# Kernel optimization log

Measured on AMD Instinct MI355X. Metric: run time of the kernel, lower is better.

## Reference

```python
import jax, jax.numpy as jnp
import numpy as np

_SIGMA = 1.5
_K1 = 0.01
_K2 = 0.03
_WINDOW_SIZE = 11
_N_CHANNELS = 3
_VALUE_RANGE = 1.0
_WEIGHTS = np.array([0.0448, 0.2856, 0.3001, 0.2363, 0.1333], dtype=np.float32)


def create_window(window_size: int, n_channels: int) -> jnp.ndarray:
    # 2D Gaussian kernel, normalized to sum 1, expanded to depthwise (C,1,ws,ws)
    coords = np.arange(window_size, dtype=np.float32) - (window_size - 1) / 2.0
    g = np.exp(-(coords ** 2) / (2.0 * _SIGMA ** 2))
    g = g / g.sum()
    k2d = np.outer(g, g).astype(np.float32)  # (ws, ws), sums to 1
    window = np.broadcast_to(k2d[None, None], (n_channels, 1, window_size, window_size))
    return jnp.asarray(window)


def _dwconv(x, window):
    # depthwise valid conv, NCHW / OIHW
    c = x.shape[1]
    return jax.lax.conv_general_dilated(
        x, window, window_strides=(1, 1), padding='VALID',
        dimension_numbers=('NCHW', 'OIHW', 'NCHW'), feature_group_count=c)


def _avg_pool2(x):
    # torch F.avg_pool2d(kernel=2, stride=2, padding=(H%2, W%2), count_include_pad=True)
    ph = x.shape[-2] % 2
    pw = x.shape[-1] % 2
    s = jax.lax.reduce_window(
        x, 0.0, jax.lax.add, window_dimensions=(1, 1, 2, 2),
        window_strides=(1, 1, 2, 2), padding=((0, 0), (0, 0), (ph, ph), (pw, pw)))
    return s * 0.25


def ssim_per_channel(x, y, window, value_range):
    mu_x = _dwconv(x, window)
    mu_y = _dwconv(y, window)
    mu_x_sq = mu_x ** 2
    mu_y_sq = mu_y ** 2
    mu_xy = mu_x * mu_y
    sigma_x_sq = _dwconv(x * x, window) - mu_x_sq
    sigma_y_sq = _dwconv(y * y, window) - mu_y_sq
    sigma_xy = _dwconv(x * y, window) - mu_xy
    c1 = (_K1 * value_range) ** 2
    c2 = (_K2 * value_range) ** 2
    cs_map = (2.0 * sigma_xy + c2) / (sigma_x_sq + sigma_y_sq + c2)
    ssim_map = (2.0 * mu_xy + c1) / (mu_x_sq + mu_y_sq + c1) * cs_map
    return ssim_map.mean(axis=(-1, -2)), cs_map.mean(axis=(-1, -2))  # (N, C) each


def msssim_per_channel(x, y, window, weights, value_range):
    n_scales = weights.shape[0]
    mcs = []
    for i in range(n_scales):
        if i > 0:
            x = _avg_pool2(x)
            y = _avg_pool2(y)
        ssim_val, cs = ssim_per_channel(x, y, window, value_range)
        mcs.append(jax.nn.relu(cs))
    stacked = jnp.stack(mcs[:-1] + [ssim_val], axis=0)  # (M, N, C)
    stacked = stacked ** weights[:, None, None]
    return jnp.prod(stacked, axis=0)  # (N, C)


def setup_inputs() -> dict:
    key = jax.random.key(0)
    k1, k2 = jax.random.split(key)
    N, C, H, W = 16, 3, 512, 512
    x = jax.random.uniform(k1, (N, C, H, W), dtype=jnp.float32)
    # target correlated with input (realistic distorted-image pair)
    noise = jax.random.uniform(k2, (N, C, H, W), dtype=jnp.float32)
    y = jnp.clip(0.9 * x + 0.1 * noise, 0.0, 1.0)
    window = create_window(_WINDOW_SIZE, _N_CHANNELS)
    weights = jnp.asarray(_WEIGHTS)
    return {"x": x, "y": y, "window": window, "weights": weights}


def reference(x, y, window, weights):
    l = msssim_per_channel(x, y, window, weights, _VALUE_RANGE).mean(axis=-1)  # (N,)
    return l.mean()  # reduction='mean' -> scalar
```

## Files before the change

### kernel.cpp

```cpp
#include <hip/hip_runtime.h>

#define HALO 10
#define SWD 76

typedef float v2f __attribute__((ext_vector_type(2)));

#define G0 0.00102838f
#define G1 0.00759871f
#define G2 0.03600077f
#define G3 0.10936069f
#define G4 0.21300556f
#define G5 0.26601176f
#define G6 G4
#define G7 G3
#define G8 G2
#define G9 G1
#define G10 G0

#define HT(QA, QB, W0, W1)                                          \
    { v2f p0; p0.x = QA.x; p0.y = QB.x;                              \
      hm += p0 * (W0); hs += p0 * p0 * (W0); hc += QA.x * QB.x * (W0);\
      v2f p1; p1.x = QA.y; p1.y = QB.y;                              \
      hm += p1 * (W1); hs += p1 * p1 * (W1); hc += QA.y * QB.y * (W1); }

__global__ __launch_bounds__(256, 3) void ssim_wave_kernel(
    const float* __restrict__ x, const float* __restrict__ y,
    float* __restrict__ xo, float* __restrict__ yo,
    float* __restrict__ acc, int H, int W, int ROWS, int do_pool)
{
    const int OH = H - HALO, OW = W - HALO;
    const int nc = blockIdx.z;
    const int tid = threadIdx.x;
    const int wave = tid >> 6, lane = tid & 63;
    const int col0 = blockIdx.x * 64;
    const int r0 = (blockIdx.y * 4 + wave) * ROWS;

    const int c = col0 + lane;
    const bool colvalid = (c < OW);
    const int cl = min(c, W - 1);
    const int chalo = min(col0 + 64 + lane, W - 1);

    const int n_out = min(ROWS, OH - r0);
    const int poolrows = do_pool ? min(ROWS, H - r0) : 0;
    const int n_iter = max(n_out > 0 ? n_out + HALO : 0, poolrows);

    const float* xp = x + (size_t)nc * H * W;
    const float* yp = y + (size_t)nc * H * W;

    __shared__ float sA[4][SWD];
    __shared__ float sB[4][SWD];
    float* myA = sA[wave];
    float* myB = sB[wave];

    const int par = lane & 1;
    const float w2_0  = par ? 0.f : G0;
    const float w2_1  = par ? G0  : G1;
    const float w2_2  = par ? G1  : G2;
    const float w2_3  = par ? G2  : G3;
    const float w2_4  = par ? G3  : G4;
    const float w2_5  = par ? G4  : G5;
    const float w2_6  = par ? G5  : G6;
    const float w2_7  = par ? G6  : G7;
    const float w2_8  = par ? G7  : G8;
    const float w2_9  = par ? G8  : G9;
    const float w2_10 = par ? G9  : G10;
    const float w2_11 = par ? G10 : 0.f;
    const int e = lane & ~1;

    v2f Hm0={0.f,0.f}, Hm1=Hm0, Hm2=Hm0, Hm3=Hm0, Hm4=Hm0, Hm5=Hm0,
        Hm6=Hm0, Hm7=Hm0, Hm8=Hm0, Hm9=Hm0, Hm10=Hm0;
    v2f Hs0=Hm0, Hs1=Hm0, Hs2=Hm0, Hs3=Hm0, Hs4=Hm0, Hs5=Hm0,
        Hs6=Hm0, Hs7=Hm0, Hs8=Hm0, Hs9=Hm0, Hs10=Hm0;
    float Hc0=0.f, Hc1=0.f, Hc2=0.f, Hc3=0.f, Hc4=0.f, Hc5=0.f,
          Hc6=0.f, Hc7=0.f, Hc8=0.f, Hc9=0.f, Hc10=0.f;

    float ssim_sum = 0.f, cs_sum = 0.f;

    float ax = 0.f, ay = 0.f, ahx = 0.f, ahy = 0.f;
    float bx = 0.f, by = 0.f, bhx = 0.f, bhy = 0.f;
    float prevx = 0.f, prevy = 0.f;

    const int Wo = W >> 1;
    float* xop = xo + (size_t)nc * (H >> 1) * Wo + (col0 >> 1);
    float* yop = yo + (size_t)nc * (H >> 1) * Wo + (col0 >> 1);

    if (n_iter > 0) {
        {
            const float* rx = xp + (size_t)r0 * W;
            const float* ry = yp + (size_t)r0 * W;
            ax = rx[cl]; ay = ry[cl];
            if (lane < HALO) { ahx = rx[chalo]; ahy = ry[chalo]; }
            const int r1 = min(r0 + 1, H - 1);
            const float* rx1 = xp + (size_t)r1 * W;
            const float* ry1 = yp + (size_t)r1 * W;
            bx = rx1[cl]; by = ry1[cl];
            if (lane < HALO) { bhx = rx1[chalo]; bhy = ry1[chalo]; }
        }
        const int NI = ((n_iter + 10) / 11) * 11;
        for (int ii = 0; ii < NI; ii += 11) {
#pragma unroll
            for (int u = 0; u < 11; ++u) {
                const int i = ii + u;

                if (do_pool && i < poolrows) {
                    float sx2 = ax + __shfl_xor(ax, 1, 64);
                    float sy2 = ay + __shfl_xor(ay, 1, 64);
                    if (i & 1) {
                        if (par == 0) {
                            const int pr = (r0 + i) >> 1;
                            xop[(size_t)pr * Wo + (lane >> 1)] = 0.25f * (prevx + sx2);
                            yop[(size_t)pr * Wo + (lane >> 1)] = 0.25f * (prevy + sy2);
                        }
                    } else { prevx = sx2; prevy = sy2; }
                }

                myA[lane] = ax; myB[lane] = ay;
                if (lane < HALO) { myA[64 + lane] = ahx; myB[64 + lane] = ahy; }

                {
                    const int rr = min(r0 + i + 2, H - 1);
                    const float* rx = xp + (size_t)rr * W;
                    const float* ry = yp + (size_t)rr * W;
                    ax = rx[cl]; ay = ry[cl];
                    if (lane < HALO) { ahx = rx[chalo]; ahy = ry[chalo]; }
                }

                const v2f* pa = (const v2f*)&myA[e];
                const v2f* pb = (const v2f*)&myB[e];
                const v2f qa0 = pa[0], qa1 = pa[1], qa2 = pa[2],
                          qa3 = pa[3], qa4 = pa[4], qa5 = pa[5];
                const v2f qb0 = pb[0], qb1 = pb[1], qb2 = pb[2],
                          qb3 = pb[3], qb4 = pb[4], qb5 = pb[5];
                v2f hm = {0.f, 0.f}, hs = {0.f, 0.f};
                float hc = 0.f;
                HT(qa0, qb0, w2_0,  w2_1)
                HT(qa1, qb1, w2_2,  w2_3)
                HT(qa2, qb2, w2_4,  w2_5)
                HT(qa3, qb3, w2_6,  w2_7)
                HT(qa4, qb4, w2_8,  w2_9)
                HT(qa5, qb5, w2_10, w2_11)

                Hm0=Hm1; Hm1=Hm2; Hm2=Hm3; Hm3=Hm4; Hm4=Hm5; Hm5=Hm6;
                Hm6=Hm7; Hm7=Hm8; Hm8=Hm9; Hm9=Hm10; Hm10=hm;
                Hs0=Hs1; Hs1=Hs2; Hs2=Hs3; Hs3=Hs4; Hs4=Hs5; Hs5=Hs6;
                Hs6=Hs7; Hs7=Hs8; Hs8=Hs9; Hs9=Hs10; Hs10=hs;
                Hc0=Hc1; Hc1=Hc2; Hc2=Hc3; Hc3=Hc4; Hc4=Hc5; Hc5=Hc6;
                Hc6=Hc7; Hc7=Hc8; Hc8=Hc9; Hc9=Hc10; Hc10=hc;

                const int o = i - HALO;
                if (o >= 0 && o < n_out && colvalid) {
                    v2f vm = Hm0*G0; vm += Hm1*G1; vm += Hm2*G2; vm += Hm3*G3;
                    vm += Hm4*G4; vm += Hm5*G5; vm += Hm6*G6; vm += Hm7*G7;
                    vm += Hm8*G8; vm += Hm9*G9; vm += Hm10*G10;
                    v2f vs = Hs0*G0; vs += Hs1*G1; vs += Hs2*G2; vs += Hs3*G3;
                    vs += Hs4*G4; vs += Hs5*G5; vs += Hs6*G6; vs += Hs7*G7;
                    vs += Hs8*G8; vs += Hs9*G9; vs += Hs10*G10;
                    float vc = Hc0*G0; vc += Hc1*G1; vc += Hc2*G2; vc += Hc3*G3;
                    vc += Hc4*G4; vc += Hc5*G5; vc += Hc6*G6; vc += Hc7*G7;
                    vc += Hc8*G8; vc += Hc9*G9; vc += Hc10*G10;

                    const float mx = vm.x, my = vm.y;
                    const float mu_x2 = mx * mx, mu_y2 = my * my, mu_xy = mx * my;
                    const float sxq = vs.x - mu_x2, syq = vs.y - mu_y2, sxyv = vc - mu_xy;
                    const float c1 = 1e-4f, c2 = 9e-4f;
                    const float cs = (2.f * sxyv + c2) * __builtin_amdgcn_rcpf(sxq + syq + c2);
                    const float ssim = (2.f * mu_xy + c1) * __builtin_amdgcn_rcpf(mu_x2 + mu_y2 + c1) * cs;
                    ssim_sum += ssim;
                    cs_sum += cs;
                }

                {
                    float t;
                    t = ax;  ax = bx;   bx = t;
                    t = ay;  ay = by;   by = t;
                    t = ahx; ahx = bhx; bhx = t;
                    t = ahy; ahy = bhy; bhy = t;
                }
            }
        }
    }

#pragma unroll
    for (int off = 32; off > 0; off >>= 1) {
        ssim_sum += __shfl_down(ssim_sum, off, 64);
        cs_sum   += __shfl_down(cs_sum,   off, 64);
    }
    if (lane == 0) {
        atomicAdd(&acc[nc * 2 + 0], ssim_sum);
        atomicAdd(&acc[nc * 2 + 1], cs_sum);
    }
}

__global__ void finalize_kernel(const float* __restrict__ acc,
                                const float* __restrict__ weights,
                                float* __restrict__ out)
{
    int t = threadIdx.x;
    float v = 0.f;
    if (t < 48) {
        float prod = 1.f;
#pragma unroll
        for (int s = 0; s < 5; ++s) {
            int O = (512 >> s) - HALO;
            float inv = 1.f / ((float)O * (float)O);
            float ssim = acc[s * 96 + t * 2 + 0] * inv;
            float cs   = acc[s * 96 + t * 2 + 1] * inv;
            float val = (s < 4) ? fmaxf(cs, 0.f) : ssim;
            prod *= powf(val, weights[s]);
        }
        v = prod;
    }
#pragma unroll
    for (int off = 32; off > 0; off >>= 1) v += __shfl_down(v, off, 64);
    if (t == 0) out[0] = v * (1.f / 48.f);
}

extern "C" void kernel_launch(void* const* d_in, const int* in_sizes, int n_in,
                              void* d_out, int out_size, void* d_ws, size_t ws_size,
                              hipStream_t stream) {
    const float* x = (const float*)d_in[0];
    const float* y = (const float*)d_in[1];
    const float* weights = (const float*)d_in[3];
    float* out = (float*)d_out;
    float* ws = (float*)d_ws;

    float* acc = ws;
    float* xs1 = ws + 512;
    float* ys1 = xs1 + (size_t)48 * 256 * 256;
    float* xs2 = ys1 + (size_t)48 * 256 * 256;
    float* ys2 = xs2 + (size_t)48 * 128 * 128;
    float* xs3 = ys2 + (size_t)48 * 128 * 128;
    float* ys3 = xs3 + (size_t)48 * 64 * 64;
    float* xs4 = ys3 + (size_t)48 * 64 * 64;
    float* ys4 = xs4 + (size_t)48 * 32 * 32;

    hipMemsetAsync(acc, 0, 480 * sizeof(float), stream);

    dim3 blk(256);
    ssim_wave_kernel<<<dim3(8, 2, 48), blk, 0, stream>>>(x, y, xs1, ys1, acc + 0 * 96, 512, 512, 64, 1);
    ssim_wave_kernel<<<dim3(4, 2, 48), blk, 0, stream>>>(xs1, ys1, xs2, ys2, acc + 1 * 96, 256, 256, 32, 1);
    ssim_wave_kernel<<<dim3(2, 2, 48), blk, 0, stream>>>(xs2, ys2, xs3, ys3, acc + 2 * 96, 128, 128, 16, 1);
    ssim_wave_kernel<<<dim3(1, 2, 48), blk, 0, stream>>>(xs3, ys3, xs4, ys4, acc + 3 * 96, 64, 64, 8, 1);
    ssim_wave_kernel<<<dim3(1, 1, 48), blk, 0, stream>>>(xs4, ys4, nullptr, nullptr, acc + 4 * 96, 32, 32, 8, 0);

    finalize_kernel<<<dim3(1), dim3(64), 0, stream>>>(acc, weights, out);
}
```

Before: 275.2 us.

## Filter sum/difference images instead of x, y and x*y separately

Changes variables to u=x+y and v=x-y, so that the five Gaussian-filtered moments collapse to four: mean and second moment of u and v. mu_x*mu_y and sigma_xy come from (a^2-b^2)/4 and (E[u^2]-E[v^2])/4. Shared memory now holds interleaved (u,v) pairs, and the horizontal pass drops the separate cross-product accumulator and its vertical history. In exchange there is extra cancellation in the subtractions, which may cost some float precision.

```diff
diff --git a/kernel.cpp b/kernel.cpp
--- a/kernel.cpp
+++ b/kernel.cpp
@@ -1,7 +1,7 @@
 #include <hip/hip_runtime.h>
 
 #define HALO 10
-#define SWD 76
+#define NPAIR 76
 
 typedef float v2f __attribute__((ext_vector_type(2)));
 
@@ -17,11 +17,7 @@
 #define G9 G1
 #define G10 G0
 
-#define HT(QA, QB, W0, W1)                                          \
-    { v2f p0; p0.x = QA.x; p0.y = QB.x;                              \
-      hm += p0 * (W0); hs += p0 * p0 * (W0); hc += QA.x * QB.x * (W0);\
-      v2f p1; p1.x = QA.y; p1.y = QB.y;                              \
-      hm += p1 * (W1); hs += p1 * p1 * (W1); hc += QA.y * QB.y * (W1); }
+#define HTAP(Q, GW)  { hm += (Q) * (GW); hs += ((Q) * (Q)) * (GW); }
 
 __global__ __launch_bounds__(256, 3) void ssim_wave_kernel(
     const float* __restrict__ x, const float* __restrict__ y,
@@ -47,32 +43,13 @@
     const float* xp = x + (size_t)nc * H * W;
     const float* yp = y + (size_t)nc * H * W;
 
-    __shared__ float sA[4][SWD];
-    __shared__ float sB[4][SWD];
-    float* myA = sA[wave];
-    float* myB = sB[wave];
-
-    const int par = lane & 1;
-    const float w2_0  = par ? 0.f : G0;
-    const float w2_1  = par ? G0  : G1;
-    const float w2_2  = par ? G1  : G2;
-    const float w2_3  = par ? G2  : G3;
-    const float w2_4  = par ? G3  : G4;
-    const float w2_5  = par ? G4  : G5;
-    const float w2_6  = par ? G5  : G6;
-    const float w2_7  = par ? G6  : G7;
-    const float w2_8  = par ? G7  : G8;
-    const float w2_9  = par ? G8  : G9;
-    const float w2_10 = par ? G9  : G10;
-    const float w2_11 = par ? G10 : 0.f;
-    const int e = lane & ~1;
+    __shared__ v2f sUD[4][NPAIR];
+    v2f* myUD = sUD[wave];
 
     v2f Hm0={0.f,0.f}, Hm1=Hm0, Hm2=Hm0, Hm3=Hm0, Hm4=Hm0, Hm5=Hm0,
         Hm6=Hm0, Hm7=Hm0, Hm8=Hm0, Hm9=Hm0, Hm10=Hm0;
     v2f Hs0=Hm0, Hs1=Hm0, Hs2=Hm0, Hs3=Hm0, Hs4=Hm0, Hs5=Hm0,
         Hs6=Hm0, Hs7=Hm0, Hs8=Hm0, Hs9=Hm0, Hs10=Hm0;
-    float Hc0=0.f, Hc1=0.f, Hc2=0.f, Hc3=0.f, Hc4=0.f, Hc5=0.f,
-          Hc6=0.f, Hc7=0.f, Hc8=0.f, Hc9=0.f, Hc10=0.f;
 
     float ssim_sum = 0.f, cs_sum = 0.f;
 
@@ -83,6 +60,7 @@
     const int Wo = W >> 1;
     float* xop = xo + (size_t)nc * (H >> 1) * Wo + (col0 >> 1);
     float* yop = yo + (size_t)nc * (H >> 1) * Wo + (col0 >> 1);
+    const int par = lane & 1;
 
     if (n_iter > 0) {
         {
@@ -114,8 +92,14 @@
                     } else { prevx = sx2; prevy = sy2; }
                 }
 
-                myA[lane] = ax; myB[lane] = ay;
-                if (lane < HALO) { myA[64 + lane] = ahx; myB[64 + lane] = ahy; }
+                {
+                    v2f ud; ud.x = ax + ay; ud.y = ax - ay;
+                    myUD[lane] = ud;
+                    if (lane < HALO) {
+                        v2f hh; hh.x = ahx + ahy; hh.y = ahx - ahy;
+                        myUD[64 + lane] = hh;
+                    }
+                }
 
                 {
                     const int rr = min(r0 + i + 2, H - 1);
@@ -125,27 +109,19 @@
                     if (lane < HALO) { ahx = rx[chalo]; ahy = ry[chalo]; }
                 }
 
-                const v2f* pa = (const v2f*)&myA[e];
-                const v2f* pb = (const v2f*)&myB[e];
-                const v2f qa0 = pa[0], qa1 = pa[1], qa2 = pa[2],
-                          qa3 = pa[3], qa4 = pa[4], qa5 = pa[5];
-                const v2f qb0 = pb[0], qb1 = pb[1], qb2 = pb[2],
-                          qb3 = pb[3], qb4 = pb[4], qb5 = pb[5];
+                const v2f* pq = myUD + lane;
+                const v2f q0 = pq[0], q1 = pq[1], q2 = pq[2], q3 = pq[3],
+                          q4 = pq[4], q5 = pq[5], q6 = pq[6], q7 = pq[7],
+                          q8 = pq[8], q9 = pq[9], q10 = pq[10];
                 v2f hm = {0.f, 0.f}, hs = {0.f, 0.f};
-                float hc = 0.f;
-                HT(qa0, qb0, w2_0,  w2_1)
-                HT(qa1, qb1, w2_2,  w2_3)
-                HT(qa2, qb2, w2_4,  w2_5)
-                HT(qa3, qb3, w2_6,  w2_7)
-                HT(qa4, qb4, w2_8,  w2_9)
-                HT(qa5, qb5, w2_10, w2_11)
+                HTAP(q0, G0)  HTAP(q1, G1)  HTAP(q2, G2)  HTAP(q3, G3)
+                HTAP(q4, G4)  HTAP(q5, G5)  HTAP(q6, G6)  HTAP(q7, G7)
+                HTAP(q8, G8)  HTAP(q9, G9)  HTAP(q10, G10)
 
                 Hm0=Hm1; Hm1=Hm2; Hm2=Hm3; Hm3=Hm4; Hm4=Hm5; Hm5=Hm6;
                 Hm6=Hm7; Hm7=Hm8; Hm8=Hm9; Hm9=Hm10; Hm10=hm;
                 Hs0=Hs1; Hs1=Hs2; Hs2=Hs3; Hs3=Hs4; Hs4=Hs5; Hs5=Hs6;
                 Hs6=Hs7; Hs7=Hs8; Hs8=Hs9; Hs9=Hs10; Hs10=hs;
-                Hc0=Hc1; Hc1=Hc2; Hc2=Hc3; Hc3=Hc4; Hc4=Hc5; Hc5=Hc6;
-                Hc6=Hc7; Hc7=Hc8; Hc8=Hc9; Hc9=Hc10; Hc10=hc;
 
                 const int o = i - HALO;
                 if (o >= 0 && o < n_out && colvalid) {
@@ -155,16 +131,16 @@
                     v2f vs = Hs0*G0; vs += Hs1*G1; vs += Hs2*G2; vs += Hs3*G3;
                     vs += Hs4*G4; vs += Hs5*G5; vs += Hs6*G6; vs += Hs7*G7;
                     vs += Hs8*G8; vs += Hs9*G9; vs += Hs10*G10;
-                    float vc = Hc0*G0; vc += Hc1*G1; vc += Hc2*G2; vc += Hc3*G3;
-                    vc += Hc4*G4; vc += Hc5*G5; vc += Hc6*G6; vc += Hc7*G7;
-                    vc += Hc8*G8; vc += Hc9*G9; vc += Hc10*G10;
-
-                    const float mx = vm.x, my = vm.y;
-                    const float mu_x2 = mx * mx, mu_y2 = my * my, mu_xy = mx * my;
-                    const float sxq = vs.x - mu_x2, syq = vs.y - mu_y2, sxyv = vc - mu_xy;
+
+                    const float A = vm.x, B = vm.y;
+                    const float a2 = A * A, b2 = B * B;
+                    const float mu_xy = 0.25f * (a2 - b2);
+                    const float msum  = 0.5f  * (a2 + b2);
+                    const float sig_s  = 0.5f  * (vs.x + vs.y) - msum;
+                    const float sig_xy = 0.25f * (vs.x - vs.y) - mu_xy;
                     const float c1 = 1e-4f, c2 = 9e-4f;
-                    const float cs = (2.f * sxyv + c2) * __builtin_amdgcn_rcpf(sxq + syq + c2);
-                    const float ssim = (2.f * mu_xy + c1) * __builtin_amdgcn_rcpf(mu_x2 + mu_y2 + c1) * cs;
+                    const float cs = (2.f * sig_xy + c2) * __builtin_amdgcn_rcpf(sig_s + c2);
+                    const float ssim = (2.f * mu_xy + c1) * __builtin_amdgcn_rcpf(msum + c1) * cs;
                     ssim_sum += ssim;
                     cs_sum += cs;
                 }
```

Measured after the change: 256.9 us. 6.7% less time.

## Filter sum and difference images to cut the convolved channels from five to four

Applied to the files above, without the earlier changes.

Instead of convolving x, y, x^2, y^2 and xy separately, the kernel stores u=x+y and d=x-y in shared memory and filters u, d, u^2 and d^2. It then recovers the means, variances and covariance algebraically. This removes one of the five convolution channels and lets the horizontal pass use packed v2f FMAs on contiguous pairs, at the cost of extra reduction adds and some loss of precision from the cancellation.

```diff
diff --git a/kernel.cpp b/kernel.cpp
--- a/kernel.cpp
+++ b/kernel.cpp
@@ -17,11 +17,9 @@
 #define G9 G1
 #define G10 G0
 
-#define HT(QA, QB, W0, W1)                                          \
-    { v2f p0; p0.x = QA.x; p0.y = QB.x;                              \
-      hm += p0 * (W0); hs += p0 * p0 * (W0); hc += QA.x * QB.x * (W0);\
-      v2f p1; p1.x = QA.y; p1.y = QB.y;                              \
-      hm += p1 * (W1); hs += p1 * p1 * (W1); hc += QA.y * QB.y * (W1); }
+#define HT2(QA, QB, WK)                                              \
+    { amu += (QA) * (WK); asu += ((QA) * (QA)) * (WK);               \
+      amd_ += (QB) * (WK); asd += ((QB) * (QB)) * (WK); }
 
 __global__ __launch_bounds__(256, 3) void ssim_wave_kernel(
     const float* __restrict__ x, const float* __restrict__ y,
@@ -65,14 +63,22 @@
     const float w2_9  = par ? G8  : G9;
     const float w2_10 = par ? G9  : G10;
     const float w2_11 = par ? G10 : 0.f;
+    v2f W0; W0.x = w2_0;  W0.y = w2_1;
+    v2f W1; W1.x = w2_2;  W1.y = w2_3;
+    v2f W2; W2.x = w2_4;  W2.y = w2_5;
+    v2f W3; W3.x = w2_6;  W3.y = w2_7;
+    v2f W4; W4.x = w2_8;  W4.y = w2_9;
+    v2f W5; W5.x = w2_10; W5.y = w2_11;
     const int e = lane & ~1;
 
-    v2f Hm0={0.f,0.f}, Hm1=Hm0, Hm2=Hm0, Hm3=Hm0, Hm4=Hm0, Hm5=Hm0,
-        Hm6=Hm0, Hm7=Hm0, Hm8=Hm0, Hm9=Hm0, Hm10=Hm0;
-    v2f Hs0=Hm0, Hs1=Hm0, Hs2=Hm0, Hs3=Hm0, Hs4=Hm0, Hs5=Hm0,
-        Hs6=Hm0, Hs7=Hm0, Hs8=Hm0, Hs9=Hm0, Hs10=Hm0;
-    float Hc0=0.f, Hc1=0.f, Hc2=0.f, Hc3=0.f, Hc4=0.f, Hc5=0.f,
-          Hc6=0.f, Hc7=0.f, Hc8=0.f, Hc9=0.f, Hc10=0.f;
+    float Au0=0.f, Au1=0.f, Au2=0.f, Au3=0.f, Au4=0.f, Au5=0.f,
+          Au6=0.f, Au7=0.f, Au8=0.f, Au9=0.f, Au10=0.f;
+    float Ad0=0.f, Ad1=0.f, Ad2=0.f, Ad3=0.f, Ad4=0.f, Ad5=0.f,
+          Ad6=0.f, Ad7=0.f, Ad8=0.f, Ad9=0.f, Ad10=0.f;
+    float Su0=0.f, Su1=0.f, Su2=0.f, Su3=0.f, Su4=0.f, Su5=0.f,
+          Su6=0.f, Su7=0.f, Su8=0.f, Su9=0.f, Su10=0.f;
+    float Sd0=0.f, Sd1=0.f, Sd2=0.f, Sd3=0.f, Sd4=0.f, Sd5=0.f,
+          Sd6=0.f, Sd7=0.f, Sd8=0.f, Sd9=0.f, Sd10=0.f;
 
     float ssim_sum = 0.f, cs_sum = 0.f;
 
@@ -114,8 +120,11 @@
                     } else { prevx = sx2; prevy = sy2; }
                 }
 
-                myA[lane] = ax; myB[lane] = ay;
-                if (lane < HALO) { myA[64 + lane] = ahx; myB[64 + lane] = ahy; }
+                myA[lane] = ax + ay; myB[lane] = ax - ay;
+                if (lane < HALO) {
+                    myA[64 + lane] = ahx + ahy;
+                    myB[64 + lane] = ahx - ahy;
+                }
 
                 {
                     const int rr = min(r0 + i + 2, H - 1);
@@ -131,40 +140,51 @@
                           qa3 = pa[3], qa4 = pa[4], qa5 = pa[5];
                 const v2f qb0 = pb[0], qb1 = pb[1], qb2 = pb[2],
                           qb3 = pb[3], qb4 = pb[4], qb5 = pb[5];
-                v2f hm = {0.f, 0.f}, hs = {0.f, 0.f};
-                float hc = 0.f;
-                HT(qa0, qb0, w2_0,  w2_1)
-                HT(qa1, qb1, w2_2,  w2_3)
-                HT(qa2, qb2, w2_4,  w2_5)
-                HT(qa3, qb3, w2_6,  w2_7)
-                HT(qa4, qb4, w2_8,  w2_9)
-                HT(qa5, qb5, w2_10, w2_11)
-
-                Hm0=Hm1; Hm1=Hm2; Hm2=Hm3; Hm3=Hm4; Hm4=Hm5; Hm5=Hm6;
-                Hm6=Hm7; Hm7=Hm8; Hm8=Hm9; Hm9=Hm10; Hm10=hm;
-                Hs0=Hs1; Hs1=Hs2; Hs2=Hs3; Hs3=Hs4; Hs4=Hs5; Hs5=Hs6;
-                Hs6=Hs7; Hs7=Hs8; Hs8=Hs9; Hs9=Hs10; Hs10=hs;
-                Hc0=Hc1; Hc1=Hc2; Hc2=Hc3; Hc3=Hc4; Hc4=Hc5; Hc5=Hc6;
-                Hc6=Hc7; Hc7=Hc8; Hc8=Hc9; Hc9=Hc10; Hc10=hc;
+                v2f amu = {0.f, 0.f}, amd_ = {0.f, 0.f};
+                v2f asu = {0.f, 0.f}, asd = {0.f, 0.f};
+                HT2(qa0, qb0, W0)
+                HT2(qa1, qb1, W1)
+                HT2(qa2, qb2, W2)
+                HT2(qa3, qb3, W3)
+                HT2(qa4, qb4, W4)
+                HT2(qa5, qb5, W5)
+                const float hu  = amu.x + amu.y;
+                const float hd  = amd_.x + amd_.y;
+                const float hsu = asu.x + asu.y;
+                const float hsd = asd.x + asd.y;
+
+                Au0=Au1; Au1=Au2; Au2=Au3; Au3=Au4; Au4=Au5; Au5=Au6;
+                Au6=Au7; Au7=Au8; Au8=Au9; Au9=Au10; Au10=hu;
+                Ad0=Ad1; Ad1=Ad2; Ad2=Ad3; Ad3=Ad4; Ad4=Ad5; Ad5=Ad6;
+                Ad6=Ad7; Ad7=Ad8; Ad8=Ad9; Ad9=Ad10; Ad10=hd;
+                Su0=Su1; Su1=Su2; Su2=Su3; Su3=Su4; Su4=Su5; Su5=Su6;
+                Su6=Su7; Su7=Su8; Su8=Su9; Su9=Su10; Su10=hsu;
+                Sd0=Sd1; Sd1=Sd2; Sd2=Sd3; Sd3=Sd4; Sd4=Sd5; Sd5=Sd6;
+                Sd6=Sd7; Sd7=Sd8; Sd8=Sd9; Sd9=Sd10; Sd10=hsd;
 
                 const int o = i - HALO;
                 if (o >= 0 && o < n_out && colvalid) {
-                    v2f vm = Hm0*G0; vm += Hm1*G1; vm += Hm2*G2; vm += Hm3*G3;
-                    vm += Hm4*G4; vm += Hm5*G5; vm += Hm6*G6; vm += Hm7*G7;
-                    vm += Hm8*G8; vm += Hm9*G9; vm += Hm10*G10;
-                    v2f vs = Hs0*G0; vs += Hs1*G1; vs += Hs2*G2; vs += Hs3*G3;
-                    vs += Hs4*G4; vs += Hs5*G5; vs += Hs6*G6; vs += Hs7*G7;
-                    vs += Hs8*G8; vs += Hs9*G9; vs += Hs10*G10;
-                    float vc = Hc0*G0; vc += Hc1*G1; vc += Hc2*G2; vc += Hc3*G3;
-                    vc += Hc4*G4; vc += Hc5*G5; vc += Hc6*G6; vc += Hc7*G7;
-                    vc += Hc8*G8; vc += Hc9*G9; vc += Hc10*G10;
-
-                    const float mx = vm.x, my = vm.y;
-                    const float mu_x2 = mx * mx, mu_y2 = my * my, mu_xy = mx * my;
-                    const float sxq = vs.x - mu_x2, syq = vs.y - mu_y2, sxyv = vc - mu_xy;
+                    float A = Au0*G0; A += Au1*G1; A += Au2*G2; A += Au3*G3;
+                    A += Au4*G4; A += Au5*G5; A += Au6*G6; A += Au7*G7;
+                    A += Au8*G8; A += Au9*G9; A += Au10*G10;
+                    float B = Ad0*G0; B += Ad1*G1; B += Ad2*G2; B += Ad3*G3;
+                    B += Ad4*G4; B += Ad5*G5; B += Ad6*G6; B += Ad7*G7;
+                    B += Ad8*G8; B += Ad9*G9; B += Ad10*G10;
+                    float su = Su0*G0; su += Su1*G1; su += Su2*G2; su += Su3*G3;
+                    su += Su4*G4; su += Su5*G5; su += Su6*G6; su += Su7*G7;
+                    su += Su8*G8; su += Su9*G9; su += Su10*G10;
+                    float sd = Sd0*G0; sd += Sd1*G1; sd += Sd2*G2; sd += Sd3*G3;
+                    sd += Sd4*G4; sd += Sd5*G5; sd += Sd6*G6; sd += Sd7*G7;
+                    sd += Sd8*G8; sd += Sd9*G9; sd += Sd10*G10;
+
+                    const float a2 = A * A, b2 = B * B;
+                    const float mu_xy = 0.25f * (a2 - b2);
+                    const float msum  = 0.5f  * (a2 + b2);
+                    const float sig_s  = 0.5f  * (su + sd) - msum;
+                    const float sig_xy = 0.25f * (su - sd) - mu_xy;
                     const float c1 = 1e-4f, c2 = 9e-4f;
-                    const float cs = (2.f * sxyv + c2) * __builtin_amdgcn_rcpf(sxq + syq + c2);
-                    const float ssim = (2.f * mu_xy + c1) * __builtin_amdgcn_rcpf(mu_x2 + mu_y2 + c1) * cs;
+                    const float cs = (2.f * sig_xy + c2) * __builtin_amdgcn_rcpf(sig_s + c2);
+                    const float ssim = (2.f * mu_xy + c1) * __builtin_amdgcn_rcpf(msum + c1) * cs;
                     ssim_sum += ssim;
                     cs_sum += cs;
                 }
```

Result: no change. 276.3 us (+0.4%).
